# Performance work log

Measured on AMD Instinct MI355X. Metric: run time of the kernel, lower is better.

Reference implementation:

```python
import jax, jax.numpy as jnp
import numpy as np

N_NODES = 50000
N_EDGES = 800000
IN_DIM_NODE = 128
IN_DIM_EDGE = 16
OUT_DIM = 32
N_HEAD = 4


def setup_inputs() -> dict:
    key = jax.random.key(0)
    ks = jax.random.split(key, 8)
    feats_node = jax.random.normal(ks[0], (N_NODES, IN_DIM_NODE), dtype=jnp.float32)
    feats_edge = jax.random.normal(ks[1], (N_EDGES, IN_DIM_EDGE), dtype=jnp.float32)
    src = jax.random.randint(ks[2], (N_EDGES,), 0, N_NODES)
    dst = jax.random.randint(ks[3], (N_EDGES,), 0, N_NODES)
    # params: init normal(std=0.5) as in the torch module
    W_node = 0.5 * jax.random.normal(ks[4], (N_HEAD * OUT_DIM, IN_DIM_NODE), dtype=jnp.float32)
    attn_l = 0.5 * jax.random.normal(ks[5], (N_HEAD, OUT_DIM), dtype=jnp.float32)
    attn_r = 0.5 * jax.random.normal(ks[6], (N_HEAD, OUT_DIM), dtype=jnp.float32)
    attn_e = 0.5 * jax.random.normal(ks[7], (N_HEAD, IN_DIM_EDGE), dtype=jnp.float32)
    return {"feats_node": feats_node, "feats_edge": feats_edge, "src": src,
            "dst": dst, "W_node": W_node, "attn_l": attn_l, "attn_r": attn_r,
            "attn_e": attn_e}


def reference(feats_node, feats_edge, src, dst, W_node, attn_l, attn_r, attn_e):
    N = feats_node.shape[0]
    H, D = attn_l.shape
    # node projection: [N, H, D]
    feat_n = (feats_node @ W_node.T).reshape(N, H, D)
    # per-node attention logits: [N, H]
    el = jnp.einsum('nhd,hd->nh', feat_n, attn_l)
    er = jnp.einsum('nhd,hd->nh', feat_n, attn_r)
    # per-edge (edge-feature) logit: [E, H]
    ee = jnp.einsum('ef,hf->eh', feats_edge, attn_e)
    # gather logits along edges and apply leaky relu (slope 0.2)
    e = jax.nn.leaky_relu(el[src] + er[dst] + ee, negative_slope=0.2)  # [E, H]
    # edge softmax segmented by destination node (numerically stable)
    m = jax.ops.segment_max(e, dst, num_segments=N)          # [N, H]
    m = jnp.where(jnp.isfinite(m), m, 0.0)                   # guard 0-degree nodes
    e_exp = jnp.exp(e - m[dst])                               # [E, H]
    s = jax.ops.segment_sum(e_exp, dst, num_segments=N)       # [N, H]
    a = e_exp / s[dst]                                        # [E, H]
    # weighted scatter-aggregate: sum over in-edges of a * ft[src]
    msg = feat_n[src] * a[:, :, None]                          # [E, H, D]
    out = jax.ops.segment_sum(msg, dst, num_segments=N)       # [N, H, D]
    return out.reshape(N, H * D)
```

## Files before the change

### kernel.cpp

```cpp
#include <hip/hip_runtime.h>
#include <hip/hip_bf16.h>
#include <math.h>

#define NN 50000
#define NE 800000
#define SCAN_NB ((NN + 255) / 256)
#define PROJ_NBLK ((NN + 31) / 32)
#define ELR_NBLK ((NN + 31) / 32)

__global__ __launch_bounds__(256) void k_prep(const float* __restrict__ W,
                                              const float* __restrict__ al,
                                              const float* __restrict__ ar,
                                              float* __restrict__ vlr) {
    int t = threadIdx.x;
    int hlr = t >> 5;
    int k4 = t & 31;
    int h = hlr & 3;
    const float* a = (hlr & 4) ? ar : al;
    float4 acc = make_float4(0.f, 0.f, 0.f, 0.f);
    for (int d = 0; d < 32; ++d) {
        float av = a[h * 32 + d];
        float4 wv = *reinterpret_cast<const float4*>(W + (size_t)(h * 32 + d) * 128 + k4 * 4);
        acc.x += av * wv.x; acc.y += av * wv.y;
        acc.z += av * wv.z; acc.w += av * wv.w;
    }
    *reinterpret_cast<float4*>(vlr + hlr * 128 + k4 * 4) = acc;
}

__global__ __launch_bounds__(256) void k_elr(const float* __restrict__ X,
                                             const float* __restrict__ vlr,
                                             float* __restrict__ elr) {
    __shared__ float vs[8 * 128];
    int t = threadIdx.x;
    for (int i = t; i < 1024; i += 256) vs[i] = vlr[i];
    __syncthreads();
    int lane = t & 63, wave = t >> 6;
    int grp = lane >> 3;
    int j = lane & 7;
    int node = blockIdx.x * 32 + wave * 8 + grp;
    float a0 = 0.f, a1 = 0.f, a2 = 0.f, a3 = 0.f, a4 = 0.f, a5 = 0.f, a6 = 0.f, a7 = 0.f;
    if (node < NN) {
        const float4* xp = reinterpret_cast<const float4*>(X + (size_t)node * 128 + j * 16);
#pragma unroll
        for (int s = 0; s < 4; ++s) {
            float4 xv = xp[s];
            const float* vb = &vs[j * 16 + s * 4];
            float4 v0 = *reinterpret_cast<const float4*>(vb + 0 * 128);
            float4 v1 = *reinterpret_cast<const float4*>(vb + 1 * 128);
            float4 v2 = *reinterpret_cast<const float4*>(vb + 2 * 128);
            float4 v3 = *reinterpret_cast<const float4*>(vb + 3 * 128);
            float4 v4 = *reinterpret_cast<const float4*>(vb + 4 * 128);
            float4 v5 = *reinterpret_cast<const float4*>(vb + 5 * 128);
            float4 v6 = *reinterpret_cast<const float4*>(vb + 6 * 128);
            float4 v7 = *reinterpret_cast<const float4*>(vb + 7 * 128);
            a0 += xv.x * v0.x + xv.y * v0.y + xv.z * v0.z + xv.w * v0.w;
            a1 += xv.x * v1.x + xv.y * v1.y + xv.z * v1.z + xv.w * v1.w;
            a2 += xv.x * v2.x + xv.y * v2.y + xv.z * v2.z + xv.w * v2.w;
            a3 += xv.x * v3.x + xv.y * v3.y + xv.z * v3.z + xv.w * v3.w;
            a4 += xv.x * v4.x + xv.y * v4.y + xv.z * v4.z + xv.w * v4.w;
            a5 += xv.x * v5.x + xv.y * v5.y + xv.z * v5.z + xv.w * v5.w;
            a6 += xv.x * v6.x + xv.y * v6.y + xv.z * v6.z + xv.w * v6.w;
            a7 += xv.x * v7.x + xv.y * v7.y + xv.z * v7.z + xv.w * v7.w;
        }
    }
#pragma unroll
    for (int off = 1; off <= 4; off <<= 1) {
        a0 += __shfl_xor(a0, off); a1 += __shfl_xor(a1, off);
        a2 += __shfl_xor(a2, off); a3 += __shfl_xor(a3, off);
        a4 += __shfl_xor(a4, off); a5 += __shfl_xor(a5, off);
        a6 += __shfl_xor(a6, off); a7 += __shfl_xor(a7, off);
    }
    float outv = (j == 0) ? a0 : (j == 1) ? a1 : (j == 2) ? a2 : (j == 3) ? a3
               : (j == 4) ? a4 : (j == 5) ? a5 : (j == 6) ? a6 : a7;
    if (node < NN) elr[(size_t)node * 8 + j] = outv;
}

__global__ __launch_bounds__(256) void k_proj4(const float* __restrict__ X,
                                               const float* __restrict__ W,
                                               __hip_bfloat16* __restrict__ FB) {
    __shared__ float Xs[32 * 128];
    const int t = threadIdx.x;
    const int w = t >> 6, l = t & 63;
    const int c = w * 32 + (l & 31);
    const int kh = (l >> 5) * 64;

    float4 wreg[16];
#pragma unroll
    for (int j = 0; j < 16; ++j)
        wreg[j] = *reinterpret_cast<const float4*>(W + (size_t)c * 128 + kh + j * 4);

    const int r0 = blockIdx.x * 32;
#pragma unroll
    for (int i = 0; i < 4; ++i) {
        int idx = t + i * 256;
        int rr = idx >> 5, c4 = (idx & 31) * 4;
        int r = r0 + rr;
        float4 v = make_float4(0.f, 0.f, 0.f, 0.f);
        if (r < NN) v = *reinterpret_cast<const float4*>(X + (size_t)r * 128 + c4);
        *reinterpret_cast<float4*>(&Xs[rr * 128 + c4]) = v;
    }
    __syncthreads();

#pragma unroll 2
    for (int rr = 0; rr < 32; ++rr) {
        const float4* xp = reinterpret_cast<const float4*>(&Xs[rr * 128 + kh]);
        float a0 = 0.f, a1 = 0.f, a2 = 0.f, a3 = 0.f;
#pragma unroll
        for (int j = 0; j < 16; ++j) {
            float4 x = xp[j];
            a0 += x.x * wreg[j].x; a1 += x.y * wreg[j].y;
            a2 += x.z * wreg[j].z; a3 += x.w * wreg[j].w;
        }
        float tot = (a0 + a1) + (a2 + a3);
        tot += __shfl_xor(tot, 32);
        int row = r0 + rr;
        if (l < 32 && row < NN) FB[(size_t)row * 128 + c] = __float2bfloat16(tot);
    }
}

__global__ void k_hist(const int* __restrict__ dst, int* __restrict__ count) {
    int e = blockIdx.x * 256 + threadIdx.x;
    if (e < NE) atomicAdd(&count[dst[e]], 1);
}

__global__ __launch_bounds__(256) void k_scan_a(const int* __restrict__ count,
                                                int* __restrict__ pre,
                                                int* __restrict__ bsum) {
    __shared__ int buf[256];
    int t = threadIdx.x;
    int gid = blockIdx.x * 256 + t;
    int v = (gid < NN) ? count[gid] : 0;
    int x = v;
    buf[t] = x;
    __syncthreads();
    for (int off = 1; off < 256; off <<= 1) {
        int add = (t >= off) ? buf[t - off] : 0;
        __syncthreads();
        x += add;
        buf[t] = x;
        __syncthreads();
    }
    if (gid < NN) pre[gid] = x - v;
    if (t == 255) bsum[blockIdx.x] = x;
}

__global__ __launch_bounds__(256) void k_scan_b(const int* __restrict__ bsum,
                                                int* __restrict__ bofs) {
    __shared__ int buf[256];
    int t = threadIdx.x;
    int v = (t < SCAN_NB) ? bsum[t] : 0;
    int x = v;
    buf[t] = x;
    __syncthreads();
    for (int off = 1; off < 256; off <<= 1) {
        int add = (t >= off) ? buf[t - off] : 0;
        __syncthreads();
        x += add;
        buf[t] = x;
        __syncthreads();
    }
    if (t < SCAN_NB) bofs[t] = x - v;
    if (t == 255) bofs[SCAN_NB] = x;
}

__global__ __launch_bounds__(256) void k_scan_c(int* __restrict__ pre,
                                                const int* __restrict__ bofs,
                                                int* __restrict__ cursor) {
    int gid = blockIdx.x * 256 + threadIdx.x;
    if (gid < NN) {
        int val = pre[gid] + bofs[gid >> 8];
        pre[gid] = val;
        cursor[gid] = val;
    }
    if (gid == 0) pre[NN] = bofs[SCAN_NB];
}

__global__ void k_logits_fill(const float* __restrict__ FE, const int* __restrict__ src,
                              const int* __restrict__ dst, const float* __restrict__ ae,
                              const float* __restrict__ elr, int* __restrict__ cursor,
                              float4* __restrict__ lsort, int* __restrict__ ssort) {
    int e = blockIdx.x * 256 + threadIdx.x;
    if (e >= NE) return;
    float fe[16];
#pragma unroll
    for (int i = 0; i < 4; ++i) {
        float4 v = *reinterpret_cast<const float4*>(FE + (size_t)e * 16 + i * 4);
        fe[i * 4 + 0] = v.x; fe[i * 4 + 1] = v.y; fe[i * 4 + 2] = v.z; fe[i * 4 + 3] = v.w;
    }
    int s = src[e], d = dst[e];
    float4 elv = *reinterpret_cast<const float4*>(elr + (size_t)s * 8);
    float4 erv = *reinterpret_cast<const float4*>(elr + (size_t)d * 8 + 4);
    float base[4] = {elv.x + erv.x, elv.y + erv.y, elv.z + erv.z, elv.w + erv.w};
    float o[4];
#pragma unroll
    for (int h = 0; h < 4; ++h) {
        float ee = 0.f;
#pragma unroll
        for (int i = 0; i < 16; ++i) ee += fe[i] * ae[h * 16 + i];
        float v = base[h] + ee;
        o[h] = v > 0.f ? v : 0.2f * v;
    }
    int pos = atomicAdd(&cursor[d], 1);
    lsort[pos] = make_float4(o[0], o[1], o[2], o[3]);
    ssort[pos] = s;
}

__global__ __launch_bounds__(256) void k_aggr4(
    const __hip_bfloat16* __restrict__ FB, const float* __restrict__ lsf,
    const int* __restrict__ ssort, const int* __restrict__ row_ptr,
    float* __restrict__ out)
{
    __shared__ float wex[4][64 * 4];
    int wid = threadIdx.x >> 6, lane = threadIdx.x & 63;
    int node = blockIdx.x * 4 + wid;
    if (node >= NN) return;
    int s0 = row_ptr[node], s1 = row_ptr[node + 1];
    int q = lane & 15, p = lane >> 4;
    float4* o4 = reinterpret_cast<float4*>(out + (size_t)node * 128);
    if (s1 == s0) {
        if (p == 0) {
            o4[2 * q]     = make_float4(0.f, 0.f, 0.f, 0.f);
            o4[2 * q + 1] = make_float4(0.f, 0.f, 0.f, 0.f);
        }
        return;
    }
    const float4* lsort = reinterpret_cast<const float4*>(lsf);
    const int deg = s1 - s0;
    const bool small = deg <= 64;

    bool have = (s0 + lane) < s1;
    float4 my = have ? lsort[s0 + lane] : make_float4(-1e30f, -1e30f, -1e30f, -1e30f);
    float m0 = my.x, m1 = my.y, m2 = my.z, m3 = my.w;
    for (int i = s0 + lane + 64; i < s1; i += 64) {
        float4 lg = lsort[i];
        m0 = fmaxf(m0, lg.x); m1 = fmaxf(m1, lg.y);
        m2 = fmaxf(m2, lg.z); m3 = fmaxf(m3, lg.w);
    }
#pragma unroll
    for (int off = 32; off; off >>= 1) {
        m0 = fmaxf(m0, __shfl_xor(m0, off)); m1 = fmaxf(m1, __shfl_xor(m1, off));
        m2 = fmaxf(m2, __shfl_xor(m2, off)); m3 = fmaxf(m3, __shfl_xor(m3, off));
    }
    float t0 = have ? __expf(my.x - m0) : 0.f;
    float t1 = have ? __expf(my.y - m1) : 0.f;
    float t2 = have ? __expf(my.z - m2) : 0.f;
    float t3 = have ? __expf(my.w - m3) : 0.f;
    if (small && have)
        *reinterpret_cast<float4*>(&wex[wid][lane * 4]) = make_float4(t0, t1, t2, t3);
    float u0 = t0, u1 = t1, u2 = t2, u3 = t3;
    for (int i = s0 + lane + 64; i < s1; i += 64) {
        float4 lg = lsort[i];
        u0 += __expf(lg.x - m0); u1 += __expf(lg.y - m1);
        u2 += __expf(lg.z - m2); u3 += __expf(lg.w - m3);
    }
#pragma unroll
    for (int off = 32; off; off >>= 1) {
        u0 += __shfl_xor(u0, off); u1 += __shfl_xor(u1, off);
        u2 += __shfl_xor(u2, off); u3 += __shfl_xor(u3, off);
    }

    int ha = q >> 2;
    float mh = (ha == 0) ? m0 : (ha == 1) ? m1 : (ha == 2) ? m2 : m3;
    float sh = (ha == 0) ? u0 : (ha == 1) ? u1 : (ha == 2) ? u2 : u3;
    float rh = 1.f / sh;
    const unsigned short* FBu = reinterpret_cast<const unsigned short*>(FB);
    float c0 = 0.f, c1 = 0.f, c2 = 0.f, c3 = 0.f, c4 = 0.f, c5 = 0.f, c6 = 0.f, c7 = 0.f;
    if (small) {
        asm volatile("s_waitcnt lgkmcnt(0)" ::: "memory");
        for (int it = s0; it < s1; it += 8) {
            int i0 = it + p, i1 = it + 4 + p;
            bool b0 = i0 < s1, b1 = i1 < s1;
            int sv0 = b0 ? ssort[i0] : 0;
            int sv1 = b1 ? ssort[i1] : 0;
            uint4 f0 = b0 ? *reinterpret_cast<const uint4*>(FBu + (size_t)sv0 * 128 + q * 8)
                          : make_uint4(0, 0, 0, 0);
            uint4 f1 = b1 ? *reinterpret_cast<const uint4*>(FBu + (size_t)sv1 * 128 + q * 8)
                          : make_uint4(0, 0, 0, 0);
            float w0 = b0 ? wex[wid][(i0 - s0) * 4 + ha] * rh : 0.f;
            float w1 = b1 ? wex[wid][(i1 - s0) * 4 + ha] * rh : 0.f;
            c0 += w0 * __uint_as_float(f0.x << 16) + w1 * __uint_as_float(f1.x << 16);
            c1 += w0 * __uint_as_float(f0.x & 0xffff0000u) + w1 * __uint_as_float(f1.x & 0xffff0000u);
            c2 += w0 * __uint_as_float(f0.y << 16) + w1 * __uint_as_float(f1.y << 16);
            c3 += w0 * __uint_as_float(f0.y & 0xffff0000u) + w1 * __uint_as_float(f1.y & 0xffff0000u);
            c4 += w0 * __uint_as_float(f0.z << 16) + w1 * __uint_as_float(f1.z << 16);
            c5 += w0 * __uint_as_float(f0.z & 0xffff0000u) + w1 * __uint_as_float(f1.z & 0xffff0000u);
            c6 += w0 * __uint_as_float(f0.w << 16) + w1 * __uint_as_float(f1.w << 16);
            c7 += w0 * __uint_as_float(f0.w & 0xffff0000u) + w1 * __uint_as_float(f1.w & 0xffff0000u);
        }
    } else {
        for (int it = s0; it < s1; it += 4) {
            int i = it + p;
            if (i < s1) {
                int sv = ssort[i];
                float lg = lsf[(size_t)i * 4 + ha];
                float wgt = __expf(lg - mh) * rh;
                uint4 f = *reinterpret_cast<const uint4*>(FBu + (size_t)sv * 128 + q * 8);
                c0 += wgt * __uint_as_float(f.x << 16);
                c1 += wgt * __uint_as_float(f.x & 0xffff0000u);
                c2 += wgt * __uint_as_float(f.y << 16);
                c3 += wgt * __uint_as_float(f.y & 0xffff0000u);
                c4 += wgt * __uint_as_float(f.z << 16);
                c5 += wgt * __uint_as_float(f.z & 0xffff0000u);
                c6 += wgt * __uint_as_float(f.w << 16);
                c7 += wgt * __uint_as_float(f.w & 0xffff0000u);
            }
        }
    }
#pragma unroll
    for (int off = 16; off <= 32; off <<= 1) {
        c0 += __shfl_xor(c0, off); c1 += __shfl_xor(c1, off);
        c2 += __shfl_xor(c2, off); c3 += __shfl_xor(c3, off);
        c4 += __shfl_xor(c4, off); c5 += __shfl_xor(c5, off);
        c6 += __shfl_xor(c6, off); c7 += __shfl_xor(c7, off);
    }
    if (p == 0) {
        o4[2 * q]     = make_float4(c0, c1, c2, c3);
        o4[2 * q + 1] = make_float4(c4, c5, c6, c7);
    }
}

extern "C" void kernel_launch(void* const* d_in, const int* in_sizes, int n_in,
                              void* d_out, int out_size, void* d_ws, size_t ws_size,
                              hipStream_t stream) {
    const float* feats_node = (const float*)d_in[0];
    const float* feats_edge = (const float*)d_in[1];
    const int*   src        = (const int*)d_in[2];
    const int*   dst        = (const int*)d_in[3];
    const float* W          = (const float*)d_in[4];
    const float* al         = (const float*)d_in[5];
    const float* ar         = (const float*)d_in[6];
    const float* ae         = (const float*)d_in[7];
    float* out = (float*)d_out;

    char* ws = (char*)d_ws;
    size_t off = 0;
    __hip_bfloat16* feat_b = (__hip_bfloat16*)(ws + off); off += (size_t)NN * 128 * 2;
    float* elr    = (float*)(ws + off); off += (size_t)NN * 8 * 4;
    float* vlr    = (float*)(ws + off); off += (size_t)8 * 128 * 4;
    float* lsort  = (float*)(ws + off); off += (size_t)NE * 4 * 4;
    int* ssort    = (int*)(ws + off);   off += (size_t)NE * 4;
    int* count    = (int*)(ws + off);   off += (size_t)NN * 4;
    int* row_ptr  = (int*)(ws + off);   off += (size_t)(NN + 16) * 4;
    int* cursor   = (int*)(ws + off);   off += (size_t)NN * 4;
    int* bsum     = (int*)(ws + off);   off += (size_t)(SCAN_NB + 16) * 4;
    int* bofs     = (int*)(ws + off);   off += (size_t)(SCAN_NB + 16) * 4;

    hipMemsetAsync(count, 0, (size_t)NN * 4, stream);

    k_hist<<<(NE + 255) / 256, 256, 0, stream>>>(dst, count);
    k_scan_a<<<SCAN_NB, 256, 0, stream>>>(count, row_ptr, bsum);
    k_scan_b<<<1, 256, 0, stream>>>(bsum, bofs);
    k_scan_c<<<SCAN_NB, 256, 0, stream>>>(row_ptr, bofs, cursor);
    k_prep<<<1, 256, 0, stream>>>(W, al, ar, vlr);
    k_elr<<<ELR_NBLK, 256, 0, stream>>>(feats_node, vlr, elr);
    k_proj4<<<PROJ_NBLK, 256, 0, stream>>>(feats_node, W, feat_b);
    k_logits_fill<<<(NE + 255) / 256, 256, 0, stream>>>(feats_edge, src, dst, ae, elr,
                                                        cursor, (float4*)lsort, ssort);
    k_aggr4<<<(NN + 3) / 4, 256, 0, stream>>>(feat_b, lsort, ssort, row_ptr, out);
}
```

Baseline: 304.5 us.

## Compute edge logits in unsorted order and gather via CSR edge-index list

Edge logits are now computed in the histogram pass and stored in original edge order, and the fill pass writes only an edge-id permutation. This removes the scattered 16-byte logit and source-index writes from the fill kernel. In exchange, the aggregation kernel gathers logits and sources indirectly through the permutation, adding random reads. The small-degree path also caches source ids in shared memory and unrolls the feature gather to four edges per step.

```diff
diff --git a/kernel.cpp b/kernel.cpp
--- a/kernel.cpp
+++ b/kernel.cpp
@@ -118,9 +118,33 @@
     }
 }
 
-__global__ void k_hist(const int* __restrict__ dst, int* __restrict__ count) {
+__global__ void k_logits_hist(const float* __restrict__ FE, const int* __restrict__ src,
+                              const int* __restrict__ dst, const float* __restrict__ ae,
+                              const float* __restrict__ elr, float4* __restrict__ logits4,
+                              int* __restrict__ count) {
     int e = blockIdx.x * 256 + threadIdx.x;
-    if (e < NE) atomicAdd(&count[dst[e]], 1);
+    if (e >= NE) return;
+    float fe[16];
+#pragma unroll
+    for (int i = 0; i < 4; ++i) {
+        float4 v = *reinterpret_cast<const float4*>(FE + (size_t)e * 16 + i * 4);
+        fe[i * 4 + 0] = v.x; fe[i * 4 + 1] = v.y; fe[i * 4 + 2] = v.z; fe[i * 4 + 3] = v.w;
+    }
+    int s = src[e], d = dst[e];
+    float4 elv = *reinterpret_cast<const float4*>(elr + (size_t)s * 8);
+    float4 erv = *reinterpret_cast<const float4*>(elr + (size_t)d * 8 + 4);
+    float base[4] = {elv.x + erv.x, elv.y + erv.y, elv.z + erv.z, elv.w + erv.w};
+    float o[4];
+#pragma unroll
+    for (int h = 0; h < 4; ++h) {
+        float ee = 0.f;
+#pragma unroll
+        for (int i = 0; i < 16; ++i) ee += fe[i] * ae[h * 16 + i];
+        float v = base[h] + ee;
+        o[h] = v > 0.f ? v : 0.2f * v;
+    }
+    logits4[e] = make_float4(o[0], o[1], o[2], o[3]);
+    atomicAdd(&count[d], 1);
 }
 
 __global__ __launch_bounds__(256) void k_scan_a(const int* __restrict__ count,
@@ -175,42 +199,22 @@
     if (gid == 0) pre[NN] = bofs[SCAN_NB];
 }
 
-__global__ void k_logits_fill(const float* __restrict__ FE, const int* __restrict__ src,
-                              const int* __restrict__ dst, const float* __restrict__ ae,
-                              const float* __restrict__ elr, int* __restrict__ cursor,
-                              float4* __restrict__ lsort, int* __restrict__ ssort) {
+__global__ void k_fill(const int* __restrict__ dst, int* __restrict__ cursor,
+                       int* __restrict__ edge_list) {
     int e = blockIdx.x * 256 + threadIdx.x;
     if (e >= NE) return;
-    float fe[16];
-#pragma unroll
-    for (int i = 0; i < 4; ++i) {
-        float4 v = *reinterpret_cast<const float4*>(FE + (size_t)e * 16 + i * 4);
-        fe[i * 4 + 0] = v.x; fe[i * 4 + 1] = v.y; fe[i * 4 + 2] = v.z; fe[i * 4 + 3] = v.w;
-    }
-    int s = src[e], d = dst[e];
-    float4 elv = *reinterpret_cast<const float4*>(elr + (size_t)s * 8);
-    float4 erv = *reinterpret_cast<const float4*>(elr + (size_t)d * 8 + 4);
-    float base[4] = {elv.x + erv.x, elv.y + erv.y, elv.z + erv.z, elv.w + erv.w};
-    float o[4];
-#pragma unroll
-    for (int h = 0; h < 4; ++h) {
-        float ee = 0.f;
-#pragma unroll
-        for (int i = 0; i < 16; ++i) ee += fe[i] * ae[h * 16 + i];
-        float v = base[h] + ee;
-        o[h] = v > 0.f ? v : 0.2f * v;
-    }
+    int d = dst[e];
     int pos = atomicAdd(&cursor[d], 1);
-    lsort[pos] = make_float4(o[0], o[1], o[2], o[3]);
-    ssort[pos] = s;
-}
-
-__global__ __launch_bounds__(256) void k_aggr4(
-    const __hip_bfloat16* __restrict__ FB, const float* __restrict__ lsf,
-    const int* __restrict__ ssort, const int* __restrict__ row_ptr,
-    float* __restrict__ out)
+    edge_list[pos] = e;
+}
+
+__global__ __launch_bounds__(256) void k_aggr5(
+    const __hip_bfloat16* __restrict__ FB, const float* __restrict__ lg4,
+    const int* __restrict__ srcv, const int* __restrict__ edge_list,
+    const int* __restrict__ row_ptr, float* __restrict__ out)
 {
     __shared__ float wex[4][64 * 4];
+    __shared__ int   sE[4][64];
     int wid = threadIdx.x >> 6, lane = threadIdx.x & 63;
     int node = blockIdx.x * 4 + wid;
     if (node >= NN) return;
@@ -224,17 +228,21 @@
         }
         return;
     }
-    const float4* lsort = reinterpret_cast<const float4*>(lsf);
+    const float4* lgf4 = reinterpret_cast<const float4*>(lg4);
     const int deg = s1 - s0;
     const bool small = deg <= 64;
 
-    bool have = (s0 + lane) < s1;
-    float4 my = have ? lsort[s0 + lane] : make_float4(-1e30f, -1e30f, -1e30f, -1e30f);
+    bool have = lane < deg;
+    int e = have ? edge_list[s0 + lane] : 0;
+    int sv = have ? srcv[e] : 0;
+    float4 my = have ? lgf4[e] : make_float4(-1e30f, -1e30f, -1e30f, -1e30f);
     float m0 = my.x, m1 = my.y, m2 = my.z, m3 = my.w;
-    for (int i = s0 + lane + 64; i < s1; i += 64) {
-        float4 lg = lsort[i];
-        m0 = fmaxf(m0, lg.x); m1 = fmaxf(m1, lg.y);
-        m2 = fmaxf(m2, lg.z); m3 = fmaxf(m3, lg.w);
+    if (!small) {
+        for (int i = s0 + lane + 64; i < s1; i += 64) {
+            float4 lg = lgf4[edge_list[i]];
+            m0 = fmaxf(m0, lg.x); m1 = fmaxf(m1, lg.y);
+            m2 = fmaxf(m2, lg.z); m3 = fmaxf(m3, lg.w);
+        }
     }
 #pragma unroll
     for (int off = 32; off; off >>= 1) {
@@ -245,13 +253,17 @@
     float t1 = have ? __expf(my.y - m1) : 0.f;
     float t2 = have ? __expf(my.z - m2) : 0.f;
     float t3 = have ? __expf(my.w - m3) : 0.f;
-    if (small && have)
+    if (small && have) {
         *reinterpret_cast<float4*>(&wex[wid][lane * 4]) = make_float4(t0, t1, t2, t3);
+        sE[wid][lane] = sv;
+    }
     float u0 = t0, u1 = t1, u2 = t2, u3 = t3;
-    for (int i = s0 + lane + 64; i < s1; i += 64) {
-        float4 lg = lsort[i];
-        u0 += __expf(lg.x - m0); u1 += __expf(lg.y - m1);
-        u2 += __expf(lg.z - m2); u3 += __expf(lg.w - m3);
+    if (!small) {
+        for (int i = s0 + lane + 64; i < s1; i += 64) {
+            float4 lg = lgf4[edge_list[i]];
+            u0 += __expf(lg.x - m0); u1 += __expf(lg.y - m1);
+            u2 += __expf(lg.z - m2); u3 += __expf(lg.w - m3);
+        }
     }
 #pragma unroll
     for (int off = 32; off; off >>= 1) {
@@ -267,34 +279,51 @@
     float c0 = 0.f, c1 = 0.f, c2 = 0.f, c3 = 0.f, c4 = 0.f, c5 = 0.f, c6 = 0.f, c7 = 0.f;
     if (small) {
         asm volatile("s_waitcnt lgkmcnt(0)" ::: "memory");
-        for (int it = s0; it < s1; it += 8) {
-            int i0 = it + p, i1 = it + 4 + p;
-            bool b0 = i0 < s1, b1 = i1 < s1;
-            int sv0 = b0 ? ssort[i0] : 0;
-            int sv1 = b1 ? ssort[i1] : 0;
-            uint4 f0 = b0 ? *reinterpret_cast<const uint4*>(FBu + (size_t)sv0 * 128 + q * 8)
+        for (int it = 0; it < deg; it += 16) {
+            int i0 = it + p, i1 = it + 4 + p, i2 = it + 8 + p, i3 = it + 12 + p;
+            bool b0 = i0 < deg, b1 = i1 < deg, b2 = i2 < deg, b3 = i3 < deg;
+            int v0 = b0 ? sE[wid][i0] : 0;
+            int v1 = b1 ? sE[wid][i1] : 0;
+            int v2 = b2 ? sE[wid][i2] : 0;
+            int v3 = b3 ? sE[wid][i3] : 0;
+            uint4 f0 = b0 ? *reinterpret_cast<const uint4*>(FBu + (size_t)v0 * 128 + q * 8)
                           : make_uint4(0, 0, 0, 0);
-            uint4 f1 = b1 ? *reinterpret_cast<const uint4*>(FBu + (size_t)sv1 * 128 + q * 8)
+            uint4 f1 = b1 ? *reinterpret_cast<const uint4*>(FBu + (size_t)v1 * 128 + q * 8)
                           : make_uint4(0, 0, 0, 0);
-            float w0 = b0 ? wex[wid][(i0 - s0) * 4 + ha] * rh : 0.f;
-            float w1 = b1 ? wex[wid][(i1 - s0) * 4 + ha] * rh : 0.f;
-            c0 += w0 * __uint_as_float(f0.x << 16) + w1 * __uint_as_float(f1.x << 16);
-            c1 += w0 * __uint_as_float(f0.x & 0xffff0000u) + w1 * __uint_as_float(f1.x & 0xffff0000u);
-            c2 += w0 * __uint_as_float(f0.y << 16) + w1 * __uint_as_float(f1.y << 16);
-            c3 += w0 * __uint_as_float(f0.y & 0xffff0000u) + w1 * __uint_as_float(f1.y & 0xffff0000u);
-            c4 += w0 * __uint_as_float(f0.z << 16) + w1 * __uint_as_float(f1.z << 16);
-            c5 += w0 * __uint_as_float(f0.z & 0xffff0000u) + w1 * __uint_as_float(f1.z & 0xffff0000u);
-            c6 += w0 * __uint_as_float(f0.w << 16) + w1 * __uint_as_float(f1.w << 16);
-            c7 += w0 * __uint_as_float(f0.w & 0xffff0000u) + w1 * __uint_as_float(f1.w & 0xffff0000u);
+            uint4 f2 = b2 ? *reinterpret_cast<const uint4*>(FBu + (size_t)v2 * 128 + q * 8)
+                          : make_uint4(0, 0, 0, 0);
+            uint4 f3 = b3 ? *reinterpret_cast<const uint4*>(FBu + (size_t)v3 * 128 + q * 8)
+                          : make_uint4(0, 0, 0, 0);
+            float w0 = b0 ? wex[wid][i0 * 4 + ha] * rh : 0.f;
+            float w1 = b1 ? wex[wid][i1 * 4 + ha] * rh : 0.f;
+            float w2 = b2 ? wex[wid][i2 * 4 + ha] * rh : 0.f;
+            float w3 = b3 ? wex[wid][i3 * 4 + ha] * rh : 0.f;
+            c0 += w0 * __uint_as_float(f0.x << 16) + w1 * __uint_as_float(f1.x << 16)
+                + w2 * __uint_as_float(f2.x << 16) + w3 * __uint_as_float(f3.x << 16);
+            c1 += w0 * __uint_as_float(f0.x & 0xffff0000u) + w1 * __uint_as_float(f1.x & 0xffff0000u)
+                + w2 * __uint_as_float(f2.x & 0xffff0000u) + w3 * __uint_as_float(f3.x & 0xffff0000u);
+            c2 += w0 * __uint_as_float(f0.y << 16) + w1 * __uint_as_float(f1.y << 16)
+                + w2 * __uint_as_float(f2.y << 16) + w3 * __uint_as_float(f3.y << 16);
+            c3 += w0 * __uint_as_float(f0.y & 0xffff0000u) + w1 * __uint_as_float(f1.y & 0xffff0000u)
+                + w2 * __uint_as_float(f2.y & 0xffff0000u) + w3 * __uint_as_float(f3.y & 0xffff0000u);
+            c4 += w0 * __uint_as_float(f0.z << 16) + w1 * __uint_as_float(f1.z << 16)
+                + w2 * __uint_as_float(f2.z << 16) + w3 * __uint_as_float(f3.z << 16);
+            c5 += w0 * __uint_as_float(f0.z & 0xffff0000u) + w1 * __uint_as_float(f1.z & 0xffff0000u)
+                + w2 * __uint_as_float(f2.z & 0xffff0000u) + w3 * __uint_as_float(f3.z & 0xffff0000u);
+            c6 += w0 * __uint_as_float(f0.w << 16) + w1 * __uint_as_float(f1.w << 16)
+                + w2 * __uint_as_float(f2.w << 16) + w3 * __uint_as_float(f3.w << 16);
+            c7 += w0 * __uint_as_float(f0.w & 0xffff0000u) + w1 * __uint_as_float(f1.w & 0xffff0000u)
+                + w2 * __uint_as_float(f2.w & 0xffff0000u) + w3 * __uint_as_float(f3.w & 0xffff0000u);
         }
     } else {
         for (int it = s0; it < s1; it += 4) {
             int i = it + p;
             if (i < s1) {
-                int sv = ssort[i];
-                float lg = lsf[(size_t)i * 4 + ha];
+                int ee = edge_list[i];
+                int sv2 = srcv[ee];
+                float lg = lg4[(size_t)ee * 4 + ha];
                 float wgt = __expf(lg - mh) * rh;
-                uint4 f = *reinterpret_cast<const uint4*>(FBu + (size_t)sv * 128 + q * 8);
+                uint4 f = *reinterpret_cast<const uint4*>(FBu + (size_t)sv2 * 128 + q * 8);
                 c0 += wgt * __uint_as_float(f.x << 16);
                 c1 += wgt * __uint_as_float(f.x & 0xffff0000u);
                 c2 += wgt * __uint_as_float(f.y << 16);
@@ -337,8 +366,8 @@
     __hip_bfloat16* feat_b = (__hip_bfloat16*)(ws + off); off += (size_t)NN * 128 * 2;
     float* elr    = (float*)(ws + off); off += (size_t)NN * 8 * 4;
     float* vlr    = (float*)(ws + off); off += (size_t)8 * 128 * 4;
-    float* lsort  = (float*)(ws + off); off += (size_t)NE * 4 * 4;
-    int* ssort    = (int*)(ws + off);   off += (size_t)NE * 4;
+    float* logits = (float*)(ws + off); off += (size_t)NE * 4 * 4;
+    int* edge_list= (int*)(ws + off);   off += (size_t)NE * 4;
     int* count    = (int*)(ws + off);   off += (size_t)NN * 4;
     int* row_ptr  = (int*)(ws + off);   off += (size_t)(NN + 16) * 4;
     int* cursor   = (int*)(ws + off);   off += (size_t)NN * 4;
@@ -347,14 +376,14 @@
 
     hipMemsetAsync(count, 0, (size_t)NN * 4, stream);
 
-    k_hist<<<(NE + 255) / 256, 256, 0, stream>>>(dst, count);
+    k_prep<<<1, 256, 0, stream>>>(W, al, ar, vlr);
+    k_elr<<<ELR_NBLK, 256, 0, stream>>>(feats_node, vlr, elr);
+    k_logits_hist<<<(NE + 255) / 256, 256, 0, stream>>>(feats_edge, src, dst, ae, elr,
+                                                        (float4*)logits, count);
     k_scan_a<<<SCAN_NB, 256, 0, stream>>>(count, row_ptr, bsum);
     k_scan_b<<<1, 256, 0, stream>>>(bsum, bofs);
     k_scan_c<<<SCAN_NB, 256, 0, stream>>>(row_ptr, bofs, cursor);
-    k_prep<<<1, 256, 0, stream>>>(W, al, ar, vlr);
-    k_elr<<<ELR_NBLK, 256, 0, stream>>>(feats_node, vlr, elr);
     k_proj4<<<PROJ_NBLK, 256, 0, stream>>>(feats_node, W, feat_b);
-    k_logits_fill<<<(NE + 255) / 256, 256, 0, stream>>>(feats_edge, src, dst, ae, elr,
-                                                        cursor, (float4*)lsort, ssort);
-    k_aggr4<<<(NN + 3) / 4, 256, 0, stream>>>(feat_b, lsort, ssort, row_ptr, out);
-}
+    k_fill<<<(NE + 255) / 256, 256, 0, stream>>>(dst, cursor, edge_list);
+    k_aggr5<<<(NN + 3) / 4, 256, 0, stream>>>(feat_b, logits, src, edge_list, row_ptr, out);
+}
```

After: 312.2 us. 1.03x slower.
